# Optimization experiments

Measured on AMD Instinct MI355X. Metric: run time of the kernel, lower is better.

## Reference

```python
import jax, jax.numpy as jnp
import numpy as np
from jax import lax

EPS = 1e-12

def _l2norm(v, axis):
    n = jnp.linalg.norm(v, axis=axis, keepdims=True)
    return v / jnp.maximum(n, EPS)

def setup_inputs() -> dict:
    key = jax.random.key(0)
    k1, k2, k3 = jax.random.split(key, 3)
    C, H, W, K = 512, 192, 192, 64
    x = jax.random.normal(k1, (C, H, W), dtype=jnp.float32)
    conv_w = jax.random.normal(k2, (K, C), dtype=jnp.float32) * 0.05  # 1x1 conv, no bias (vladv2=False)
    centroids = jax.random.uniform(k3, (K, C), dtype=jnp.float32)
    return {"x": x, "conv_w": conv_w, "centroids": centroids}

def reference(x, conv_w, centroids):
    K = conv_w.shape[0]
    x4 = x[None]                      # [1,C,H,W]
    N, C, H, W = x4.shape
    L = H * W
    # descriptor-wise L2 normalization over channels
    x4 = _l2norm(x4, axis=1)
    # 1x1 conv -> soft assignment over clusters
    logits = jnp.einsum('kc,nchw->nkhw', conv_w, x4)
    soft = jax.nn.softmax(logits, axis=1)          # [N,K,H,W]
    sa_flat = soft.reshape(N, K, L)
    # top-2 cluster indices per location (argmax + second largest)
    _, top2 = lax.top_k(sa_flat.transpose(0, 2, 1), 2)  # [N,L,2]
    first, second = top2[..., 0], top2[..., 1]
    # unfold 3x3, padding 1: windows [N, L, K, 9] in (kh,kw) order
    pad = jnp.pad(soft, ((0, 0), (0, 0), (1, 1), (1, 1)))
    patches = jnp.stack([pad[:, :, di:di + H, dj:dj + W]
                         for di in range(3) for dj in range(3)], axis=2)  # [N,K,9,H,W]
    windows = patches.reshape(N, K, 9, L).transpose(0, 3, 1, 2)           # [N,L,K,9]
    # keep only windows of the top-2 clusters at each location
    karange = jnp.arange(K)[None, None, :]
    keep = (karange == first[:, :, None]) | (karange == second[:, :, None])  # [N,L,K]
    wsel = windows * keep[..., None].astype(windows.dtype)
    # fold (transpose of unfold): overlap-add back to [N,K,H,W]
    ws = wsel.transpose(0, 2, 3, 1).reshape(N, K, 9, H, W)
    out_pad = jnp.zeros((N, K, H + 2, W + 2), dtype=ws.dtype)
    t = 0
    for di in range(3):
        for dj in range(3):
            out_pad = out_pad.at[:, :, di:di + H, dj:dj + W].add(ws[:, :, t])
            t += 1
    weight = out_pad[:, :, 1:H + 1, 1:W + 1]
    # border mask: (min distance to border)^4
    ii = jnp.arange(H); jj = jnp.arange(W)
    mi = jnp.minimum(H - 1 - ii, ii)[:, None]
    mj = jnp.minimum(W - 1 - jj, jj)[None, :]
    m = jnp.minimum(mi, mj).astype(weight.dtype)
    m2 = m * m
    mask = m2 * m2
    weight = weight * mask[None, None]
    sa2 = weight.reshape(N, K, L)
    # per-cluster residual accumulation, vectorized (replaces the 64-iter loop)
    xf = x4.reshape(N, C, L)
    vlad = jnp.einsum('nkl,ncl->nkc', sa2, xf) - sa2.sum(-1)[..., None] * centroids[None]
    vlad = _l2norm(vlad, axis=2)               # intra-normalization
    v = vlad.reshape(N, -1)
    v = _l2norm(v, axis=1)
    return v
```

## Files before the change

kernel.cpp:

```cpp
#include <hip/hip_runtime.h>

#define HH 192
#define WW 192
#define LL (HH * WW)
#define CC 512
#define KK 64
#define EPSF 1e-12f
typedef unsigned long long ull;
typedef unsigned int uint;
typedef unsigned short ushort;

#define NCHUNK 192
#define CHUNKL (LL / NCHUNK)

typedef short bf16x8 __attribute__((ext_vector_type(8)));
typedef float f32x4 __attribute__((ext_vector_type(4)));

__device__ __forceinline__ void gl16(const void* g, void* l) {
    __builtin_amdgcn_global_load_lds((const __attribute__((address_space(1))) void*)g,
                                     (__attribute__((address_space(3))) void*)l, 16, 0, 0);
}

__device__ inline void split3(float v, ushort& h, ushort& md, ushort& lo) {
    uint b  = __float_as_uint(v);
    uint hb = b & 0xFFFF0000u;
    float r1 = v - __uint_as_float(hb);
    uint mb = __float_as_uint(r1) & 0xFFFF0000u;
    float r2 = r1 - __uint_as_float(mb);
    uint lb = __float_as_uint(r2) & 0xFFFF0000u;
    h = (ushort)(hb >> 16); md = (ushort)(mb >> 16); lo = (ushort)(lb >> 16);
}

__device__ inline void split2(float v, ushort& h, ushort& lo) {
    uint b  = __float_as_uint(v);
    uint hb = b & 0xFFFF0000u;
    float r = v - __uint_as_float(hb);
    h = (ushort)(hb >> 16); lo = (ushort)(__float_as_uint(r) >> 16);
}

__global__ __launch_bounds__(256) void k0_prep(const float* __restrict__ w,
                                               ushort* __restrict__ Whi,
                                               ushort* __restrict__ Wmid,
                                               ushort* __restrict__ Wlo,
                                               float* __restrict__ Szero) {
    int idx = blockIdx.x * 256 + threadIdx.x;
    int k = idx >> 9;
    int c = idx & 511;
    int s = c >> 5, w32 = c & 31, quad = w32 >> 3, j = w32 & 7;
    int kg = k >> 4, m = k & 15;
    int dst = (((s * 4 + kg) * 4 + quad) * 16 + m) * 8 + j;
    float v = w[idx];
    ushort h, md, lo;
    split3(v, h, md, lo);
    Whi[dst] = h; Wmid[dst] = md; Wlo[dst] = lo;
    if (blockIdx.x == 0 && threadIdx.x < 128) Szero[threadIdx.x] = 0.f;
}

__global__ __launch_bounds__(256) void k1_logits(const float* __restrict__ x,
                                                 const ushort* __restrict__ Whi,
                                                 const ushort* __restrict__ Wmid,
                                                 const ushort* __restrict__ Wlo,
                                                 float* __restrict__ soft,
                                                 float* __restrict__ invn,
                                                 ull* __restrict__ keep) {
    __shared__ ushort wl[2][12][512];
    __shared__ float xs[2][32][64];
    int t = threadIdx.x, lane = t & 63, wid = t >> 6;
    int m = lane & 15, quad = lane >> 4;
    int pb = blockIdx.x * 64;

    f32x4 acc[4];
#pragma unroll
    for (int kg = 0; kg < 4; ++kg) acc[kg] = (f32x4){0.f, 0.f, 0.f, 0.f};
    float ss = 0.f;

    const ushort* Wp[3] = {Whi, Wmid, Wlo};
    const float* gbase = x + (size_t)(4 * wid + quad) * LL + pb + m * 4;

    gl16(gbase, &xs[0][4 * wid][0]);
    gl16(gbase + (size_t)16 * LL, &xs[0][16 + 4 * wid][0]);
#pragma unroll
    for (int q = 0; q < 3; ++q) {
        int ch = 3 * wid + q;
        gl16(Wp[ch >> 2] + (size_t)(((0 * 4 + (ch & 3)) * 64 + lane) * 8), &wl[0][ch][(size_t)lane * 8]);
    }

    int cur = 0;
#pragma unroll
    for (int s = 0; s < 16; ++s) {
        __syncthreads();
        if (s < 15) {
            const float* g = gbase + (size_t)(s + 1) * 32 * LL;
            gl16(g, &xs[cur ^ 1][4 * wid][0]);
            gl16(g + (size_t)16 * LL, &xs[cur ^ 1][16 + 4 * wid][0]);
#pragma unroll
            for (int q = 0; q < 3; ++q) {
                int ch = 3 * wid + q;
                gl16(Wp[ch >> 2] + (size_t)((((s + 1) * 4 + (ch & 3)) * 64 + lane) * 8),
                     &wl[cur ^ 1][ch][(size_t)lane * 8]);
            }
        }
        float xv[8];
#pragma unroll
        for (int j = 0; j < 8; ++j) xv[j] = xs[cur][quad * 8 + j][wid * 16 + m];
        bf16x8 Bh, Bm, Bl;
#pragma unroll
        for (int j = 0; j < 8; ++j) {
            float v = xv[j];
            ss = fmaf(v, v, ss);
            ushort h, md, lo;
            split3(v, h, md, lo);
            Bh[j] = (short)h; Bm[j] = (short)md; Bl[j] = (short)lo;
        }
#pragma unroll
        for (int kg = 0; kg < 4; ++kg) {
            bf16x8 Ah = *(const bf16x8*)&wl[cur][kg    ][(size_t)lane * 8];
            bf16x8 Am = *(const bf16x8*)&wl[cur][4 + kg][(size_t)lane * 8];
            bf16x8 Al = *(const bf16x8*)&wl[cur][8 + kg][(size_t)lane * 8];
            f32x4 a = acc[kg];
            a = __builtin_amdgcn_mfma_f32_16x16x32_bf16(Ah, Bh, a, 0, 0, 0);
            a = __builtin_amdgcn_mfma_f32_16x16x32_bf16(Ah, Bm, a, 0, 0, 0);
            a = __builtin_amdgcn_mfma_f32_16x16x32_bf16(Am, Bh, a, 0, 0, 0);
            a = __builtin_amdgcn_mfma_f32_16x16x32_bf16(Ah, Bl, a, 0, 0, 0);
            a = __builtin_amdgcn_mfma_f32_16x16x32_bf16(Al, Bh, a, 0, 0, 0);
            a = __builtin_amdgcn_mfma_f32_16x16x32_bf16(Am, Bm, a, 0, 0, 0);
            acc[kg] = a;
        }
        cur ^= 1;
    }

    ss += __shfl_xor(ss, 16);
    ss += __shfl_xor(ss, 32);
    float iv = 1.0f / fmaxf(sqrtf(ss), EPSF);
    int px = pb + wid * 16 + m;
    if (quad == 0) invn[px] = iv;

    float lg[16];
    float M1 = -3.0e38f, M2 = -3.0e38f; int I1 = 0, I2 = 0;
#pragma unroll
    for (int kg = 0; kg < 4; ++kg)
#pragma unroll
        for (int r = 0; r < 4; ++r) {
            float v = acc[kg][r] * iv;
            lg[kg * 4 + r] = v;
            int kk = kg * 16 + quad * 4 + r;
            if (v > M1)      { M2 = M1; I2 = I1; M1 = v; I1 = kk; }
            else if (v > M2) { M2 = v; I2 = kk; }
        }
#pragma unroll
    for (int st = 0; st < 2; ++st) {
        int d = 16 << st;
        float a1 = __shfl_xor(M1, d); int b1 = __shfl_xor(I1, d);
        float a2 = __shfl_xor(M2, d); int b2 = __shfl_xor(I2, d);
        if (a1 > M1 || (a1 == M1 && b1 < I1)) { M2 = M1; I2 = I1; M1 = a1; I1 = b1; }
        else if (a1 > M2 || (a1 == M2 && b1 < I2)) { M2 = a1; I2 = b1; }
        if (a2 > M1 || (a2 == M1 && b2 < I1)) { M2 = M1; I2 = I1; M1 = a2; I1 = b2; }
        else if (a2 > M2 || (a2 == M2 && b2 < I2)) { M2 = a2; I2 = b2; }
    }

    float es = 0.f;
#pragma unroll
    for (int q = 0; q < 16; ++q) { float e = __expf(lg[q] - M1); lg[q] = e; es += e; }
    es += __shfl_xor(es, 16);
    es += __shfl_xor(es, 32);
    float rs = 1.0f / es;

    float4* sp = (float4*)(soft + (size_t)px * KK + quad * 4);
#pragma unroll
    for (int kg = 0; kg < 4; ++kg) {
        float4 o;
        o.x = lg[kg * 4 + 0] * rs; o.y = lg[kg * 4 + 1] * rs;
        o.z = lg[kg * 4 + 2] * rs; o.w = lg[kg * 4 + 3] * rs;
        sp[kg * 4] = o;
    }
    if (quad == 0) keep[px] = (1ull << I1) | (1ull << I2);
}

__global__ __launch_bounds__(256) void k2_weight(const float* __restrict__ soft,
                                                 const ull* __restrict__ keep,
                                                 const float* __restrict__ invn,
                                                 float* __restrict__ S,
                                                 ushort* __restrict__ w2t_hi,
                                                 ushort* __restrict__ w2t_lo) {
    __shared__ float sred[4][64];
    int t = threadIdx.x, lane = t & 63, wid = t >> 6;
    int l0 = blockIdx.x * 32 + wid * 8;
    float sk = 0.f;
    bf16x8 hv, lv;
#pragma unroll
    for (int p = 0; p < 8; ++p) {
        int l = l0 + p;
        int i = l / WW, j = l % WW;
        int m = min(min(i, HH - 1 - i), min(j, WW - 1 - j));
        float bm = (float)m; bm *= bm; bm *= bm;
        int cnt = 0;
#pragma unroll
        for (int di = -1; di <= 1; ++di) {
            int ii = i + di;
            if (ii < 0 || ii >= HH) continue;
#pragma unroll
            for (int dj = -1; dj <= 1; ++dj) {
                int jj = j + dj;
                if (jj < 0 || jj >= WW) continue;
                ull nb = keep[ii * WW + jj];
                cnt += (int)((nb >> lane) & 1ull);
            }
        }
        float v = soft[(size_t)l * KK + lane];
        float u = v * (float)cnt * bm;
        sk += u;
        float w2v = u * invn[l];
        ushort h, lo;
        split2(w2v, h, lo);
        hv[p] = (short)h; lv[p] = (short)lo;
    }
    size_t off = (size_t)((((l0 >> 5) * 4 + (lane >> 4)) * 64 + ((l0 >> 3) & 3) * 16 + (lane & 15)) * 8);
    *(bf16x8*)(w2t_hi + off) = hv;
    *(bf16x8*)(w2t_lo + off) = lv;
    sred[wid][lane] = sk;
    __syncthreads();
    if (wid == 0)
        atomicAdd(&S[lane], sred[0][lane] + sred[1][lane] + sred[2][lane] + sred[3][lane]);
}

__global__ __launch_bounds__(256) void k3_mfma(const ushort* __restrict__ w2t_hi,
                                               const ushort* __restrict__ w2t_lo,
                                               const float* __restrict__ x,
                                               float* __restrict__ partials) {
    int chunk = blockIdx.x;
    int c0 = blockIdx.y * 128;
    int l0 = chunk * CHUNKL;
    int t = threadIdx.x, lane = t & 63, wid = t >> 6;
    int m = lane & 15, quad = lane >> 4;

    f32x4 acc[4][2];
#pragma unroll
    for (int kg = 0; kg < 4; ++kg)
#pragma unroll
        for (int cg = 0; cg < 2; ++cg) acc[kg][cg] = (f32x4){0.f, 0.f, 0.f, 0.f};

    const float* xb = x + (size_t)(c0 + wid * 32 + m) * LL + l0 + quad * 8;

#pragma unroll
    for (int lb = 0; lb < CHUNKL; lb += 32) {
        int lstep = (l0 + lb) >> 5;
        bf16x8 Ah[4], Al[4];
#pragma unroll
        for (int kg = 0; kg < 4; ++kg) {
            size_t off = (size_t)(((lstep * 4 + kg) * 64 + lane) * 8);
            Ah[kg] = *(const bf16x8*)(w2t_hi + off);
            Al[kg] = *(const bf16x8*)(w2t_lo + off);
        }
        bf16x8 Bh[2], Bl[2];
#pragma unroll
        for (int cg = 0; cg < 2; ++cg) {
            const float* xr = xb + (size_t)(cg * 16) * LL + lb;
            float4 v0 = *(const float4*)xr;
            float4 v1 = *(const float4*)(xr + 4);
            float vv[8] = {v0.x, v0.y, v0.z, v0.w, v1.x, v1.y, v1.z, v1.w};
#pragma unroll
            for (int j = 0; j < 8; ++j) {
                ushort h, lo;
                split2(vv[j], h, lo);
                Bh[cg][j] = (short)h; Bl[cg][j] = (short)lo;
            }
        }
#pragma unroll
        for (int cg = 0; cg < 2; ++cg)
#pragma unroll
            for (int kg = 0; kg < 4; ++kg) {
                acc[kg][cg] = __builtin_amdgcn_mfma_f32_16x16x32_bf16(Ah[kg], Bh[cg], acc[kg][cg], 0, 0, 0);
                acc[kg][cg] = __builtin_amdgcn_mfma_f32_16x16x32_bf16(Ah[kg], Bl[cg], acc[kg][cg], 0, 0, 0);
                acc[kg][cg] = __builtin_amdgcn_mfma_f32_16x16x32_bf16(Al[kg], Bh[cg], acc[kg][cg], 0, 0, 0);
            }
    }
    float* pp = partials + (size_t)chunk * KK * CC;
#pragma unroll
    for (int kg = 0; kg < 4; ++kg)
#pragma unroll
        for (int cg = 0; cg < 2; ++cg) {
            int cout = c0 + wid * 32 + cg * 16 + m;
#pragma unroll
            for (int r = 0; r < 4; ++r) {
                int kout = kg * 16 + quad * 4 + r;
                pp[(size_t)kout * CC + cout] = acc[kg][cg][r];
            }
        }
}

__global__ __launch_bounds__(512) void k4a_reduce(const float* __restrict__ partials,
                                                  const float* __restrict__ S,
                                                  const float* __restrict__ cent,
                                                  float* __restrict__ vlad,
                                                  float* __restrict__ rowsq) {
    __shared__ float red[512];
    int k = blockIdx.x;
    int ci = threadIdx.x & 127;
    int c = blockIdx.y * 128 + ci;
    int q = threadIdx.x >> 7;
    const float* pk = partials + (size_t)q * (NCHUNK / 4) * KK * CC + (size_t)k * CC + c;
    float s0 = 0.f, s1 = 0.f, s2 = 0.f, s3 = 0.f;
    for (int ch = 0; ch < NCHUNK / 4; ch += 4) {
        s0 += pk[(size_t)(ch + 0) * KK * CC];
        s1 += pk[(size_t)(ch + 1) * KK * CC];
        s2 += pk[(size_t)(ch + 2) * KK * CC];
        s3 += pk[(size_t)(ch + 3) * KK * CC];
    }
    red[threadIdx.x] = (s0 + s1) + (s2 + s3);
    __syncthreads();
    float vsq = 0.f;
    if (q == 0) {
        float v = red[ci] + red[ci + 128] + red[ci + 256] + red[ci + 384];
        v -= S[k] * cent[k * CC + c];
        vlad[k * CC + c] = v;
        vsq = v * v;
    }
    __syncthreads();
    red[threadIdx.x] = vsq;
    __syncthreads();
    for (int off = 256; off > 0; off >>= 1) {
        if (threadIdx.x < off) red[threadIdx.x] += red[threadIdx.x + off];
        __syncthreads();
    }
    if (threadIdx.x == 0) atomicAdd(&rowsq[k], red[0]);
}

__global__ __launch_bounds__(256) void k4c_finish(const float* __restrict__ vlad,
                                                  const float* __restrict__ rowsq,
                                                  float* __restrict__ out) {
    __shared__ float rns[64];
    int t = threadIdx.x;
    if (t < 64) {
        float tot = rowsq[t];
        float r = 1.0f / fmaxf(sqrtf(tot), EPSF);
        float contrib = tot * r * r;
#pragma unroll
        for (int off = 32; off; off >>= 1) contrib += __shfl_xor(contrib, off, 64);
        float ginv = 1.0f / fmaxf(sqrtf(contrib), EPSF);
        rns[t] = r * ginv;
    }
    __syncthreads();
    int idx4 = blockIdx.x * 256 + t;
    int k = idx4 >> 7;
    float s = rns[k];
    float4 v = ((const float4*)vlad)[idx4];
    v.x *= s; v.y *= s; v.z *= s; v.w *= s;
    ((float4*)out)[idx4] = v;
}

extern "C" void kernel_launch(void* const* d_in, const int* in_sizes, int n_in,
                              void* d_out, int out_size, void* d_ws, size_t ws_size,
                              hipStream_t stream) {
    const float* x      = (const float*)d_in[0];
    const float* conv_w = (const float*)d_in[1];
    const float* cent   = (const float*)d_in[2];
    float* out = (float*)d_out;

    float* ws    = (float*)d_ws;
    ushort* Whi  = (ushort*)ws;
    ushort* Wmid = Whi + 32768;
    ushort* Wlo  = Wmid + 32768;
    float* soft  = ws + 49152;
    float* invn  = soft + (size_t)KK * LL;
    float* S     = invn + LL;
    float* rowsq = S + KK;
    float* vlad  = rowsq + KK;
    ull*   keep  = (ull*)(vlad + 32768);
    ushort* w2t_hi = (ushort*)(keep + LL);
    ushort* w2t_lo = w2t_hi + (size_t)LL * KK;
    float* partials = (float*)(w2t_lo + (size_t)LL * KK);

    k0_prep<<<(KK * CC) / 256, 256, 0, stream>>>(conv_w, Whi, Wmid, Wlo, S);
    k1_logits<<<LL / 64, 256, 0, stream>>>(x, Whi, Wmid, Wlo, soft, invn, keep);
    k2_weight<<<LL / 32, 256, 0, stream>>>(soft, keep, invn, S, w2t_hi, w2t_lo);
    k3_mfma<<<dim3(NCHUNK, 4), 256, 0, stream>>>(w2t_hi, w2t_lo, x, partials);
    k4a_reduce<<<dim3(KK, 4), 512, 0, stream>>>(partials, S, cent, vlad, rowsq);
    k4c_finish<<<(KK * CC / 4) / 256, 256, 0, stream>>>(vlad, rowsq, out);
}
```

Baseline: 189.1 us.

## Double-buffer weight and x tiles into LDS via async global_load_lds in k3_mfma

The MFMA kernel used to load the weight fragments and x rows straight from global memory into registers. It now stages both into double-buffered LDS tiles with global_load_lds, so the next step's loads overlap the current step's MFMAs. The x rows are placed with an XOR swizzle to avoid bank conflicts. This adds a __syncthreads per step and more LDS use, which may lower occupancy.

After: 188.0 us, median of 2. Within noise of the previous version (-0.6%).

```diff
diff --git a/kernel.cpp b/kernel.cpp
--- a/kernel.cpp
+++ b/kernel.cpp
@@ -227,9 +227,12 @@
                                                const ushort* __restrict__ w2t_lo,
                                                const float* __restrict__ x,
                                                float* __restrict__ partials) {
+    __shared__ ushort wa[2][8][512];
+    __shared__ float  xb[2][128][32];
     int chunk = blockIdx.x;
     int c0 = blockIdx.y * 128;
     int l0 = chunk * CHUNKL;
+    int lsbase = chunk * (CHUNKL / 32);
     int t = threadIdx.x, lane = t & 63, wid = t >> 6;
     int m = lane & 15, quad = lane >> 4;
 
@@ -239,24 +242,53 @@
 #pragma unroll
         for (int cg = 0; cg < 2; ++cg) acc[kg][cg] = (f32x4){0.f, 0.f, 0.f, 0.f};
 
-    const float* xb = x + (size_t)(c0 + wid * 32 + m) * LL + l0 + quad * 8;
-
-#pragma unroll
-    for (int lb = 0; lb < CHUNKL; lb += 32) {
-        int lstep = (l0 + lb) >> 5;
+    int rowg = lane >> 3, gph = lane & 7;
+    int swzl = ((gph ^ rowg) * 4);
+
+#pragma unroll
+    for (int q = 0; q < 2; ++q) {
+        int ch = 2 * wid + q;
+        const ushort* src = (ch < 4 ? w2t_hi : w2t_lo) + (size_t)(((lsbase * 4 + (ch & 3)) * 64 + lane) * 8);
+        gl16(src, &wa[0][ch][(size_t)lane * 8]);
+    }
+#pragma unroll
+    for (int i = 0; i < 4; ++i) {
+        int row = wid * 32 + 8 * i + rowg;
+        gl16(x + (size_t)(c0 + row) * LL + l0 + swzl, &xb[0][wid * 32 + 8 * i][0]);
+    }
+
+    int cur = 0;
+#pragma unroll
+    for (int st = 0; st < CHUNKL / 32; ++st) {
+        __syncthreads();
+        if (st < CHUNKL / 32 - 1) {
+#pragma unroll
+            for (int q = 0; q < 2; ++q) {
+                int ch = 2 * wid + q;
+                const ushort* src = (ch < 4 ? w2t_hi : w2t_lo) +
+                                    (size_t)((((lsbase + st + 1) * 4 + (ch & 3)) * 64 + lane) * 8);
+                gl16(src, &wa[cur ^ 1][ch][(size_t)lane * 8]);
+            }
+#pragma unroll
+            for (int i = 0; i < 4; ++i) {
+                int row = wid * 32 + 8 * i + rowg;
+                gl16(x + (size_t)(c0 + row) * LL + l0 + (st + 1) * 32 + swzl,
+                     &xb[cur ^ 1][wid * 32 + 8 * i][0]);
+            }
+        }
         bf16x8 Ah[4], Al[4];
 #pragma unroll
         for (int kg = 0; kg < 4; ++kg) {
-            size_t off = (size_t)(((lstep * 4 + kg) * 64 + lane) * 8);
-            Ah[kg] = *(const bf16x8*)(w2t_hi + off);
-            Al[kg] = *(const bf16x8*)(w2t_lo + off);
+            Ah[kg] = *(const bf16x8*)&wa[cur][kg    ][(size_t)lane * 8];
+            Al[kg] = *(const bf16x8*)&wa[cur][4 + kg][(size_t)lane * 8];
         }
         bf16x8 Bh[2], Bl[2];
 #pragma unroll
         for (int cg = 0; cg < 2; ++cg) {
-            const float* xr = xb + (size_t)(cg * 16) * LL + lb;
-            float4 v0 = *(const float4*)xr;
-            float4 v1 = *(const float4*)(xr + 4);
+            int crow = wid * 32 + cg * 16 + m;
+            const float* xr = &xb[cur][crow][0];
+            float4 v0 = *(const float4*)(xr + (((quad * 2    ) ^ (m & 7)) * 4));
+            float4 v1 = *(const float4*)(xr + (((quad * 2 + 1) ^ (m & 7)) * 4));
             float vv[8] = {v0.x, v0.y, v0.z, v0.w, v1.x, v1.y, v1.z, v1.w};
 #pragma unroll
             for (int j = 0; j < 8; ++j) {
@@ -273,6 +305,7 @@
                 acc[kg][cg] = __builtin_amdgcn_mfma_f32_16x16x32_bf16(Ah[kg], Bl[cg], acc[kg][cg], 0, 0, 0);
                 acc[kg][cg] = __builtin_amdgcn_mfma_f32_16x16x32_bf16(Al[kg], Bh[cg], acc[kg][cg], 0, 0, 0);
             }
+        cur ^= 1;
     }
     float* pp = partials + (size_t)chunk * KK * CC;
 #pragma unroll
```
